# Kernel optimization log

Measured on AMD Instinct MI355X. Metric: run time of the kernel, lower is better.

## Reference

```python
import jax, jax.numpy as jnp
import numpy as np

N_TOKENS = 1024
HIDDEN = 2048
N_EXPERTS = 16
MOE_INTER = 1024
TOP_K = 6
N_GROUP = 4
TOPK_GROUP = 2
N_SHARED = 2
ROUTED_SCALING = 2.5
RENORM = True
CAPACITY = 1024  # >> N_TOKENS*TOP_K/N_EXPERTS = 384; overflow probability negligible


def setup_inputs() -> dict:
    key = jax.random.key(0)
    ks = jax.random.split(key, 7)
    s = 0.02
    return {
        'hidden_states': jax.random.normal(ks[0], (N_TOKENS, HIDDEN), jnp.float32),
        'gate_w': jax.random.normal(ks[1], (N_EXPERTS, HIDDEN), jnp.float32) * s,
        'gate_bias': jax.random.normal(ks[2], (N_EXPERTS,), jnp.float32) * s,
        'w_gate_up': jax.random.normal(ks[3], (N_EXPERTS, HIDDEN, 2 * MOE_INTER), jnp.float32) * s,
        'w_down': jax.random.normal(ks[4], (N_EXPERTS, MOE_INTER, HIDDEN), jnp.float32) * s,
        'shared_w_gate_up': jax.random.normal(ks[5], (HIDDEN, 2 * N_SHARED * MOE_INTER), jnp.float32) * s,
        'shared_w_down': jax.random.normal(ks[6], (N_SHARED * MOE_INTER, HIDDEN), jnp.float32) * s,
    }


def _swiglu(gu):
    # npu_swiglu with activate_left=True: silu(first half) * second half
    g, u = jnp.split(gu, 2, axis=-1)
    return jax.nn.silu(g) * u


def reference(hidden_states, gate_w, gate_bias, w_gate_up, w_down, shared_w_gate_up, shared_w_down):
    x = hidden_states
    N, H = x.shape
    E, K, C = N_EXPERTS, TOP_K, CAPACITY
    P = N * K  # number of (token, slot) pairs

    # ---- MoEGate: router logits + noaux_tc grouped top-k ----
    logits = x @ gate_w.T                              # [N, E]
    scores = jax.nn.sigmoid(logits)                    # sigmoid scoring (noaux_tc)
    s_corr = scores + gate_bias[None, :]
    sg = s_corr.reshape(N, N_GROUP, E // N_GROUP)
    group_scores = jax.lax.top_k(sg, 2)[0].sum(-1)     # top-2 sum per group [N, G]
    _, gidx = jax.lax.top_k(group_scores, TOPK_GROUP)
    gmask = jnp.sum(jax.nn.one_hot(gidx, N_GROUP, dtype=jnp.float32), axis=1) > 0
    masked = jnp.where(gmask[:, :, None], sg, -jnp.inf).reshape(N, E)
    _, topk_ids = jax.lax.top_k(masked, K)             # [N, K]
    w = jnp.take_along_axis(scores, topk_ids, axis=-1)  # weights from original scores
    if RENORM:
        w = w / jnp.sum(w, axis=-1, keepdims=True)
    w = w * ROUTED_SCALING

    # ---- dispatch: fixed-capacity buffers per expert ----
    flat_e = topk_ids.reshape(P)
    onehot = jax.nn.one_hot(flat_e, E, dtype=jnp.int32)
    pos = jnp.cumsum(onehot, axis=0)[jnp.arange(P), flat_e] - 1  # slot within expert
    valid = pos < C
    buf = jnp.full((E, C), P, jnp.int32).at[flat_e, jnp.clip(pos, 0, C - 1)].set(
        jnp.where(valid, jnp.arange(P, dtype=jnp.int32), P))
    tok = jnp.where(buf < P, buf // K, N)              # token index per slot, N = pad
    x_pad = jnp.concatenate([x, jnp.zeros((1, H), x.dtype)], axis=0)
    xe = x_pad[tok]                                    # [E, C, H]

    # ---- grouped expert GEMMs (SwiGLU MLP per expert) ----
    h = jnp.einsum('ech,ehi->eci', xe, w_gate_up)      # [E, C, 2I]
    y = jnp.einsum('eci,eih->ech', _swiglu(h), w_down)  # [E, C, H]

    # ---- combine: weighted scatter-add back to tokens ----
    w_pad = jnp.concatenate([w.reshape(P), jnp.zeros((1,), w.dtype)])
    pw = w_pad[jnp.where(buf < P, buf, P)]             # [E, C]
    routed = jnp.zeros((N + 1, H), x.dtype).at[tok].add(y * pw[:, :, None])[:N]

    # ---- shared experts (reduce_results=False, fused add) ----
    shared = _swiglu(x @ shared_w_gate_up) @ shared_w_down
    return routed + shared
```

## Files before the change

### kernel.cpp

```cpp
#include <hip/hip_runtime.h>
#include <hip/hip_bf16.h>
#include <math.h>

typedef __attribute__((ext_vector_type(8))) short bf16x8;
typedef __attribute__((ext_vector_type(4))) float f32x4;

#define N_TOK 1024
#define HID   2048
#define NEXP  16
#define NE2   18
#define INTER 1024
#define TOPK  6
#define CAP   1024

__device__ __forceinline__ unsigned short f2bf(float f) {
  unsigned u = __builtin_bit_cast(unsigned, f);
  u += 0x7fffu + ((u >> 16) & 1u);
  return (unsigned short)(u >> 16);
}
__device__ __forceinline__ float b2f(short s) {
  unsigned u = ((unsigned)(unsigned short)s) << 16;
  return __builtin_bit_cast(float, u);
}
__device__ __forceinline__ void gll16(const void* g, void* l) {
  __builtin_amdgcn_global_load_lds(
      (const __attribute__((address_space(1))) unsigned int*)g,
      (__attribute__((address_space(3))) unsigned int*)l, 16, 0, 0);
}
__device__ __forceinline__ void xcd_remap(int& bx, int& by, int& bz) {
  int gx = gridDim.x, gy = gridDim.y;
  int nwg = gx * gy * (int)gridDim.z;
  int lid = bx + gx * (by + gy * bz);
  int q = nwg >> 3, r = nwg & 7;
  int xcd = lid & 7, i = lid >> 3;
  int swz = (xcd < r ? xcd * (q + 1) : r * (q + 1) + (xcd - r) * q) + i;
  bx = swz % gx; int t2 = swz / gx; by = t2 % gy; bz = t2 / gy;
}

__global__ __launch_bounds__(256) void router_k(
    const float* __restrict__ x, const float* __restrict__ gw,
    const float* __restrict__ gb, int* __restrict__ counts,
    int* __restrict__ tok_list, int* __restrict__ meta,
    float* __restrict__ pwt, unsigned short* __restrict__ x_bf)
{
  const int t   = blockIdx.x;
  const int tid = threadIdx.x;
  __shared__ float xrow[HID];
  __shared__ float logits[NEXP];

  for (int i = tid; i < HID; i += 256) {
    float v = x[(size_t)t * HID + i];
    xrow[i] = v;
    x_bf[(size_t)t * HID + i] = f2bf(v);
  }
  __syncthreads();

  const int w = tid >> 6, lane = tid & 63;
  for (int s = 0; s < 4; ++s) {
    int e = w * 4 + s;
    const float* g = gw + (size_t)e * HID;
    float p = 0.f;
    for (int i = lane; i < HID; i += 64) p += xrow[i] * g[i];
    for (int off = 32; off; off >>= 1) p += __shfl_down(p, off);
    if (lane == 0) logits[e] = p;
  }
  __syncthreads();

  if (tid == 0) {
    float sc[NEXP], scorr[NEXP];
    for (int e = 0; e < NEXP; ++e) {
      float s1 = 1.f / (1.f + expf(-logits[e]));
      sc[e] = s1; scorr[e] = s1 + gb[e];
    }
    float gs[4];
    for (int g = 0; g < 4; ++g) {
      float m1 = -1e30f, m2 = -1e30f;
      for (int j = 0; j < 4; ++j) {
        float v = scorr[g * 4 + j];
        if (v > m1) { m2 = m1; m1 = v; } else if (v > m2) m2 = v;
      }
      gs[g] = m1 + m2;
    }
    int g1 = 0;
    for (int g = 1; g < 4; ++g) if (gs[g] > gs[g1]) g1 = g;
    int g2 = -1;
    for (int g = 0; g < 4; ++g) { if (g == g1) continue; if (g2 < 0 || gs[g] > gs[g2]) g2 = g; }

    bool taken[NEXP];
    for (int e = 0; e < NEXP; ++e) taken[e] = false;
    int ids[TOPK]; float wv[TOPK]; float wsum = 0.f;
    for (int k = 0; k < TOPK; ++k) {
      int best = -1; float bv = -1e30f;
      for (int e = 0; e < NEXP; ++e) {
        int grp = e >> 2;
        if (grp != g1 && grp != g2) continue;
        if (taken[e]) continue;
        if (scorr[e] > bv) { bv = scorr[e]; best = e; }
      }
      taken[best] = true; ids[k] = best; wv[k] = sc[best]; wsum += sc[best];
    }
    float inv = 2.5f / wsum;
    for (int k = 0; k < TOPK; ++k) {
      int e = ids[k];
      int slot = atomicAdd(&counts[e], 1);
      tok_list[e * CAP + slot] = t;
      meta[t * TOPK + k] = (e << 16) | slot;
      pwt[t * TOPK + k] = wv[k] * inv;
    }
  }
}

__global__ __launch_bounds__(256) void t_gu_k(
    const float* __restrict__ wgu, const float* __restrict__ sgu,
    unsigned short* __restrict__ dst)
{
  const int z = blockIdx.z;
  const int n0 = blockIdx.x * 64, k0 = blockIdx.y * 64;
  const float* src; int ld; int cb;
  if (z < 16) { src = wgu + (size_t)z * HID * (2 * INTER); ld = 2 * INTER; cb = n0; }
  else { int j = z - 16; src = sgu; ld = 4096;
         cb = (n0 < 1024) ? j * 1024 + n0 : 1024 * j + 1024 + n0; }
  __shared__ __align__(16) unsigned short t2[64][72];
  const int tid = threadIdx.x;
  const int kb = tid >> 4, nb = tid & 15;
  unsigned short h[4][4];
  #pragma unroll
  for (int j = 0; j < 4; ++j) {
    float4 f = *(const float4*)(src + (size_t)(k0 + kb * 4 + j) * ld + cb + nb * 4);
    h[j][0] = f2bf(f.x); h[j][1] = f2bf(f.y); h[j][2] = f2bf(f.z); h[j][3] = f2bf(f.w);
  }
  #pragma unroll
  for (int i = 0; i < 4; ++i) {
    int rr = nb * 4 + i;
    unsigned lo  = h[0][i] | ((unsigned)h[1][i] << 16);
    unsigned hi2 = h[2][i] | ((unsigned)h[3][i] << 16);
    unsigned long long v = (unsigned long long)lo | ((unsigned long long)hi2 << 32);
    *(unsigned long long*)((char*)t2 + rr * 144 + ((kb * 8) ^ ((rr & 7) << 4))) = v;
  }
  __syncthreads();
  unsigned short* d = dst + (size_t)z * HID * (2 * INTER);
  #pragma unroll
  for (int i = 0; i < 2; ++i) {
    int c = tid + 256 * i;
    int nl = c >> 3, s = c & 7;
    uint4 v = *(const uint4*)((const char*)t2 + nl * 144 + ((s * 16) ^ ((nl & 7) << 4)));
    *(uint4*)(d + (size_t)(n0 + nl) * HID + k0 + s * 8) = v;
  }
}

__global__ __launch_bounds__(256) void t_d_k(
    const float* __restrict__ wd, const float* __restrict__ sd,
    unsigned short* __restrict__ dst)
{
  const int z = blockIdx.z;
  const int n0 = blockIdx.x * 64, k0 = blockIdx.y * 64;
  const float* src = (z < 16) ? wd + (size_t)z * INTER * HID
                              : sd + (size_t)(z - 16) * INTER * HID;
  __shared__ __align__(16) unsigned short t2[64][72];
  const int tid = threadIdx.x;
  const int kb = tid >> 4, nb = tid & 15;
  unsigned short h[4][4];
  #pragma unroll
  for (int j = 0; j < 4; ++j) {
    float4 f = *(const float4*)(src + (size_t)(k0 + kb * 4 + j) * HID + n0 + nb * 4);
    h[j][0] = f2bf(f.x); h[j][1] = f2bf(f.y); h[j][2] = f2bf(f.z); h[j][3] = f2bf(f.w);
  }
  #pragma unroll
  for (int i = 0; i < 4; ++i) {
    int rr = nb * 4 + i;
    unsigned lo  = h[0][i] | ((unsigned)h[1][i] << 16);
    unsigned hi2 = h[2][i] | ((unsigned)h[3][i] << 16);
    unsigned long long v = (unsigned long long)lo | ((unsigned long long)hi2 << 32);
    *(unsigned long long*)((char*)t2 + rr * 144 + ((kb * 8) ^ ((rr & 7) << 4))) = v;
  }
  __syncthreads();
  unsigned short* d = dst + (size_t)z * HID * INTER;
  #pragma unroll
  for (int i = 0; i < 2; ++i) {
    int c = tid + 256 * i;
    int nl = c >> 3, s = c & 7;
    uint4 v = *(const uint4*)((const char*)t2 + nl * 144 + ((s * 16) ^ ((nl & 7) << 4)));
    *(uint4*)(d + (size_t)(n0 + nl) * INTER + k0 + s * 8) = v;
  }
}

template<int MODE>
__global__ __launch_bounds__(256) void gemm_bf16_k(
    const unsigned short* __restrict__ A, int lda, size_t a_estride,
    const unsigned short* __restrict__ Wt, int K, size_t w_estride,
    const int* __restrict__ counts, const int* __restrict__ tok_list,
    unsigned short* __restrict__ outb, int out_ld, size_t out_estride)
{
  int bx = blockIdx.x, by = blockIdx.y, bz = blockIdx.z;
  xcd_remap(bx, by, bz);
  const int e  = bz;
  const int m0 = by * 128;
  const int M  = (e < 16) ? counts[e] : N_TOK;
  if (m0 >= M) return;
  const int n0 = bx * (MODE == 0 ? 64 : 128);

  __shared__ __align__(16) unsigned short Al[128 * 64];
  __shared__ __align__(16) unsigned short Bl[128 * 64];

  const int tid = threadIdx.x, lane = tid & 63, wid = tid >> 6;
  const int wm = wid >> 1, wn = wid & 1, l15 = lane & 15, hi = lane >> 4;

  const unsigned short* Ap = A + (size_t)e * a_estride;
  const unsigned short* Wp = Wt + (size_t)e * w_estride;

  const unsigned short* asrc[4]; void* adst[4];
  const unsigned short* bsrc[4]; void* bdst[4];
  #pragma unroll
  for (int i = 0; i < 4; ++i) {
    int c = tid + 256 * i;
    int r = c >> 3, s = c & 7, sl = s ^ (r & 7);
    int slot = m0 + r;
    int row;
    if (MODE == 0) row = (e < 16) ? ((slot < M) ? tok_list[e * CAP + slot] : 0) : slot;
    else           row = slot;
    asrc[i] = Ap + (size_t)row * lda + sl * 8;
    adst[i] = (char*)Al + c * 16;
    int nrow = (MODE == 0) ? ((r < 64) ? n0 + r : 1024 + n0 + (r - 64)) : (n0 + r);
    bsrc[i] = Wp + (size_t)nrow * K + sl * 8;
    bdst[i] = (char*)Bl + c * 16;
  }

  int bn[4];
  if (MODE == 0) { bn[0] = wn*32; bn[1] = wn*32+16; bn[2] = 64+wn*32; bn[3] = 80+wn*32; }
  else           { bn[0] = wn*64; bn[1] = wn*64+16; bn[2] = wn*64+32; bn[3] = wn*64+48; }

  f32x4 acc[4][4];
  #pragma unroll
  for (int a0 = 0; a0 < 4; ++a0)
    #pragma unroll
    for (int b0 = 0; b0 < 4; ++b0) acc[a0][b0] = (f32x4){0.f, 0.f, 0.f, 0.f};

  for (int kt = 0; kt < K; kt += 64) {
    #pragma unroll
    for (int i = 0; i < 4; ++i) gll16(asrc[i] + kt, adst[i]);
    #pragma unroll
    for (int i = 0; i < 4; ++i) gll16(bsrc[i] + kt, bdst[i]);
    __syncthreads();

    #pragma unroll
    for (int kk = 0; kk < 64; kk += 32) {
      bf16x8 af[4], bv[4];
      #pragma unroll
      for (int mi = 0; mi < 4; ++mi) {
        int r = wm * 64 + mi * 16 + l15;
        int off = (r * 128 + (kk + hi * 8) * 2) ^ ((r & 7) << 4);
        af[mi] = *(const bf16x8*)((const char*)Al + off);
      }
      #pragma unroll
      for (int ni = 0; ni < 4; ++ni) {
        int r = bn[ni] + l15;
        int off = (r * 128 + (kk + hi * 8) * 2) ^ ((r & 7) << 4);
        bv[ni] = *(const bf16x8*)((const char*)Bl + off);
      }
      #pragma unroll
      for (int mi = 0; mi < 4; ++mi)
        #pragma unroll
        for (int ni = 0; ni < 4; ++ni)
          acc[mi][ni] = __builtin_amdgcn_mfma_f32_16x16x32_bf16(af[mi], bv[ni], acc[mi][ni], 0, 0, 0);
    }
    __syncthreads();
  }

  const int rbase = hi * 4;
  if (MODE == 0) {
    #pragma unroll
    for (int mi = 0; mi < 4; ++mi)
      #pragma unroll
      for (int rr = 0; rr < 4; ++rr) {
        int slot = m0 + wm * 64 + mi * 16 + rbase + rr;
        if (slot >= M) continue;
        #pragma unroll
        for (int j = 0; j < 2; ++j) {
          float g = acc[mi][j][rr], u = acc[mi][j + 2][rr];
          float sv = g / (1.f + expf(-g)) * u;
          int col = n0 + wn * 32 + j * 16 + l15;
          outb[(size_t)e * out_estride + (size_t)slot * out_ld + col] = f2bf(sv);
        }
      }
  } else {
    #pragma unroll
    for (int mi = 0; mi < 4; ++mi)
      #pragma unroll
      for (int rr = 0; rr < 4; ++rr) {
        int slot = m0 + wm * 64 + mi * 16 + rbase + rr;
        if (slot >= M) continue;
        unsigned short* row = outb + (size_t)e * out_estride + (size_t)slot * out_ld;
        #pragma unroll
        for (int ni = 0; ni < 4; ++ni)
          row[n0 + bn[ni] + l15] = f2bf(acc[mi][ni][rr]);
      }
  }
}

__global__ __launch_bounds__(256) void combine_k(
    const unsigned short* __restrict__ ybuf, const int* __restrict__ meta,
    const float* __restrict__ pwt, float* __restrict__ out)
{
  const int t = blockIdx.x;
  const int c0 = threadIdx.x * 8;
  float acc[8];
  {
    bf16x8 v0 = *(const bf16x8*)(ybuf + ((size_t)16 * CAP + t) * HID + c0);
    bf16x8 v1 = *(const bf16x8*)(ybuf + ((size_t)17 * CAP + t) * HID + c0);
    #pragma unroll
    for (int j = 0; j < 8; ++j) acc[j] = b2f(v0[j]) + b2f(v1[j]);
  }
  #pragma unroll
  for (int k = 0; k < TOPK; ++k) {
    int m = meta[t * TOPK + k];
    float w = pwt[t * TOPK + k];
    int e = m >> 16, s = m & 0xffff;
    bf16x8 v = *(const bf16x8*)(ybuf + ((size_t)e * CAP + s) * HID + c0);
    #pragma unroll
    for (int j = 0; j < 8; ++j) acc[j] += w * b2f(v[j]);
  }
  float4* o = (float4*)(out + (size_t)t * HID + c0);
  o[0] = make_float4(acc[0], acc[1], acc[2], acc[3]);
  o[1] = make_float4(acc[4], acc[5], acc[6], acc[7]);
}

extern "C" void kernel_launch(void* const* d_in, const int* in_sizes, int n_in,
                              void* d_out, int out_size, void* d_ws, size_t ws_size,
                              hipStream_t stream) {
  const float* x   = (const float*)d_in[0];
  const float* gw  = (const float*)d_in[1];
  const float* gb  = (const float*)d_in[2];
  const float* wgu = (const float*)d_in[3];
  const float* wd  = (const float*)d_in[4];
  const float* sgu = (const float*)d_in[5];
  const float* sd  = (const float*)d_in[6];
  float* out = (float*)d_out;

  char* ws = (char*)d_ws;
  int*   counts   = (int*)ws;
  int*   tok_list = (int*)(ws + 256);
  int*   meta     = (int*)(ws + 256 + 65536);
  float* pwt      = (float*)(ws + 256 + 65536 + 24576);
  unsigned short* x_bf  = (unsigned short*)(ws + 128 * 1024);
  unsigned short* act   = x_bf + (size_t)N_TOK * HID;
  unsigned short* ybuf  = act + (size_t)NE2 * CAP * INTER;
  unsigned short* wt_gu = ybuf + (size_t)NE2 * CAP * HID;
  unsigned short* wt_d  = wt_gu + (size_t)NE2 * HID * 2 * INTER;
  const size_t need = (size_t)((char*)(wt_d + (size_t)NE2 * HID * INTER) - ws);
  if (ws_size < need) return;

  hipMemsetAsync(counts, 0, 256, stream);
  router_k<<<N_TOK, 256, 0, stream>>>(x, gw, gb, counts, tok_list, meta, pwt, x_bf);

  t_gu_k<<<dim3(2 * INTER / 64, HID / 64, NE2), 256, 0, stream>>>(wgu, sgu, wt_gu);
  t_d_k<<<dim3(HID / 64, INTER / 64, NE2), 256, 0, stream>>>(wd, sd, wt_d);

  gemm_bf16_k<0><<<dim3(INTER / 64, CAP / 128, NE2), 256, 0, stream>>>(
      x_bf, HID, 0, wt_gu, HID, (size_t)HID * 2 * INTER, counts, tok_list,
      act, INTER, (size_t)CAP * INTER);
  gemm_bf16_k<1><<<dim3(HID / 128, CAP / 128, NE2), 256, 0, stream>>>(
      act, INTER, (size_t)CAP * INTER, wt_d, INTER, (size_t)HID * INTER, counts, nullptr,
      ybuf, HID, (size_t)CAP * HID);

  combine_k<<<N_TOK, 256, 0, stream>>>(ybuf, meta, pwt, out);
}
```

Measured before the change: 478.3 us.

## Widen GEMM N-tile and double-buffer weight tiles in LDS

The grouped expert GEMMs now use a 128x256 output tile (twice as wide in N) with 32 accumulators per lane. The weight (B) tiles are double-buffered in LDS so the next tile's global-to-LDS loads overlap with MFMA work on the current one, while A is still single-buffered and reloaded after a barrier. The XCD block remapping is removed and launch bounds ask for 2 blocks per SM. The goal is more reuse of the A tile per weight load and less load latency exposed at barriers, at the cost of more LDS (about 80KB), higher register pressure, and fewer blocks in flight.

```diff
diff --git a/kernel.cpp b/kernel.cpp
--- a/kernel.cpp
+++ b/kernel.cpp
@@ -26,15 +26,6 @@
   __builtin_amdgcn_global_load_lds(
       (const __attribute__((address_space(1))) unsigned int*)g,
       (__attribute__((address_space(3))) unsigned int*)l, 16, 0, 0);
-}
-__device__ __forceinline__ void xcd_remap(int& bx, int& by, int& bz) {
-  int gx = gridDim.x, gy = gridDim.y;
-  int nwg = gx * gy * (int)gridDim.z;
-  int lid = bx + gx * (by + gy * bz);
-  int q = nwg >> 3, r = nwg & 7;
-  int xcd = lid & 7, i = lid >> 3;
-  int swz = (xcd < r ? xcd * (q + 1) : r * (q + 1) + (xcd - r) * q) + i;
-  bx = swz % gx; int t2 = swz / gx; by = t2 % gy; bz = t2 / gy;
 }
 
 __global__ __launch_bounds__(256) void router_k(
@@ -185,22 +176,20 @@
 }
 
 template<int MODE>
-__global__ __launch_bounds__(256) void gemm_bf16_k(
+__global__ __launch_bounds__(256, 2) void gemm_bf16_k(
     const unsigned short* __restrict__ A, int lda, size_t a_estride,
     const unsigned short* __restrict__ Wt, int K, size_t w_estride,
     const int* __restrict__ counts, const int* __restrict__ tok_list,
     unsigned short* __restrict__ outb, int out_ld, size_t out_estride)
 {
-  int bx = blockIdx.x, by = blockIdx.y, bz = blockIdx.z;
-  xcd_remap(bx, by, bz);
-  const int e  = bz;
-  const int m0 = by * 128;
+  const int e  = blockIdx.z;
+  const int m0 = blockIdx.y * 128;
   const int M  = (e < 16) ? counts[e] : N_TOK;
   if (m0 >= M) return;
-  const int n0 = bx * (MODE == 0 ? 64 : 128);
+  const int n0 = blockIdx.x * (MODE == 0 ? 128 : 256);
 
   __shared__ __align__(16) unsigned short Al[128 * 64];
-  __shared__ __align__(16) unsigned short Bl[128 * 64];
+  __shared__ __align__(16) unsigned short Bl[2][256 * 64];
 
   const int tid = threadIdx.x, lane = tid & 63, wid = tid >> 6;
   const int wm = wid >> 1, wn = wid & 1, l15 = lane & 15, hi = lane >> 4;
@@ -208,63 +197,98 @@
   const unsigned short* Ap = A + (size_t)e * a_estride;
   const unsigned short* Wp = Wt + (size_t)e * w_estride;
 
-  const unsigned short* asrc[4]; void* adst[4];
-  const unsigned short* bsrc[4]; void* bdst[4];
+  const int r0 = tid >> 3, s0 = tid & 7, sl = s0 ^ (r0 & 7);
+  const unsigned short* asrc[4]; int aoff[4];
   #pragma unroll
   for (int i = 0; i < 4; ++i) {
-    int c = tid + 256 * i;
-    int r = c >> 3, s = c & 7, sl = s ^ (r & 7);
+    int r = r0 + 32 * i;
     int slot = m0 + r;
     int row;
     if (MODE == 0) row = (e < 16) ? ((slot < M) ? tok_list[e * CAP + slot] : 0) : slot;
     else           row = slot;
     asrc[i] = Ap + (size_t)row * lda + sl * 8;
-    adst[i] = (char*)Al + c * 16;
-    int nrow = (MODE == 0) ? ((r < 64) ? n0 + r : 1024 + n0 + (r - 64)) : (n0 + r);
-    bsrc[i] = Wp + (size_t)nrow * K + sl * 8;
-    bdst[i] = (char*)Bl + c * 16;
-  }
-
-  int bn[4];
-  if (MODE == 0) { bn[0] = wn*32; bn[1] = wn*32+16; bn[2] = 64+wn*32; bn[3] = 80+wn*32; }
-  else           { bn[0] = wn*64; bn[1] = wn*64+16; bn[2] = wn*64+32; bn[3] = wn*64+48; }
-
-  f32x4 acc[4][4];
+    aoff[i] = (tid + 256 * i) * 16;
+  }
+  const unsigned short* bpg;
+  const unsigned short* bpu;
+  if (MODE == 0) {
+    bpg = Wp + (size_t)(n0 + r0) * K + sl * 8;
+    bpu = Wp + (size_t)(1024 + n0 + r0) * K + sl * 8;
+  } else {
+    bpg = Wp + (size_t)(n0 + r0) * K + sl * 8;
+    bpu = bpg + (size_t)128 * K;
+  }
+  const size_t bstep = (size_t)32 * K;
+
+  int bn[8];
+  #pragma unroll
+  for (int ni = 0; ni < 8; ++ni) {
+    if (MODE == 0) bn[ni] = (ni < 4) ? (wn * 64 + ni * 16) : (128 + wn * 64 + (ni - 4) * 16);
+    else           bn[ni] = wn * 128 + ni * 16;
+  }
+
+  f32x4 acc[4][8];
   #pragma unroll
   for (int a0 = 0; a0 < 4; ++a0)
     #pragma unroll
-    for (int b0 = 0; b0 < 4; ++b0) acc[a0][b0] = (f32x4){0.f, 0.f, 0.f, 0.f};
-
-  for (int kt = 0; kt < K; kt += 64) {
-    #pragma unroll
-    for (int i = 0; i < 4; ++i) gll16(asrc[i] + kt, adst[i]);
-    #pragma unroll
-    for (int i = 0; i < 4; ++i) gll16(bsrc[i] + kt, bdst[i]);
-    __syncthreads();
-
-    #pragma unroll
-    for (int kk = 0; kk < 64; kk += 32) {
-      bf16x8 af[4], bv[4];
-      #pragma unroll
-      for (int mi = 0; mi < 4; ++mi) {
-        int r = wm * 64 + mi * 16 + l15;
-        int off = (r * 128 + (kk + hi * 8) * 2) ^ ((r & 7) << 4);
-        af[mi] = *(const bf16x8*)((const char*)Al + off);
-      }
-      #pragma unroll
-      for (int ni = 0; ni < 4; ++ni) {
-        int r = bn[ni] + l15;
-        int off = (r * 128 + (kk + hi * 8) * 2) ^ ((r & 7) << 4);
-        bv[ni] = *(const bf16x8*)((const char*)Bl + off);
-      }
-      #pragma unroll
-      for (int mi = 0; mi < 4; ++mi)
-        #pragma unroll
-        for (int ni = 0; ni < 4; ++ni)
-          acc[mi][ni] = __builtin_amdgcn_mfma_f32_16x16x32_bf16(af[mi], bv[ni], acc[mi][ni], 0, 0, 0);
-    }
-    __syncthreads();
-  }
+    for (int b0 = 0; b0 < 8; ++b0) acc[a0][b0] = (f32x4){0.f, 0.f, 0.f, 0.f};
+
+  #define ISSUE_B(buf, kt)                                                  \
+    _Pragma("unroll")                                                       \
+    for (int i = 0; i < 4; ++i)                                             \
+      gll16(bpg + bstep * i + (kt), (char*)(buf) + (tid + 256 * i) * 16);   \
+    _Pragma("unroll")                                                       \
+    for (int i = 0; i < 4; ++i)                                             \
+      gll16(bpu + bstep * i + (kt), (char*)(buf) + (tid + 256 * (i + 4)) * 16);
+  #define ISSUE_A(kt)                                                       \
+    _Pragma("unroll")                                                       \
+    for (int i = 0; i < 4; ++i) gll16(asrc[i] + (kt), (char*)Al + aoff[i]);
+  #define COMPUTE(Bb)                                                       \
+    _Pragma("unroll")                                                       \
+    for (int kk = 0; kk < 64; kk += 32) {                                   \
+      bf16x8 af[4], bv[8];                                                  \
+      _Pragma("unroll")                                                     \
+      for (int mi = 0; mi < 4; ++mi) {                                      \
+        int r = wm * 64 + mi * 16 + l15;                                    \
+        int off = (r * 128 + (kk + hi * 8) * 2) ^ ((r & 7) << 4);           \
+        af[mi] = *(const bf16x8*)((const char*)Al + off);                   \
+      }                                                                     \
+      _Pragma("unroll")                                                     \
+      for (int ni = 0; ni < 8; ++ni) {                                      \
+        int r = bn[ni] + l15;                                               \
+        int off = (r * 128 + (kk + hi * 8) * 2) ^ ((r & 7) << 4);           \
+        bv[ni] = *(const bf16x8*)((const char*)(Bb) + off);                 \
+      }                                                                     \
+      _Pragma("unroll")                                                     \
+      for (int mi = 0; mi < 4; ++mi)                                        \
+        _Pragma("unroll")                                                   \
+        for (int ni = 0; ni < 8; ++ni)                                      \
+          acc[mi][ni] = __builtin_amdgcn_mfma_f32_16x16x32_bf16(            \
+              af[mi], bv[ni], acc[mi][ni], 0, 0, 0);                        \
+    }
+
+  const int nt = K >> 6;
+  ISSUE_B(Bl[0], 0)
+  ISSUE_A(0)
+  asm volatile("s_waitcnt vmcnt(0)" ::: "memory");
+  __builtin_amdgcn_s_barrier();
+
+  int p = 0;
+  for (int t = 0; t < nt; ++t) {
+    const bool pf = (t + 1 < nt);
+    if (pf) { ISSUE_B(Bl[p ^ 1], (t + 1) << 6) }
+    COMPUTE(Bl[p])
+    __builtin_amdgcn_s_barrier();
+    if (pf) {
+      ISSUE_A((t + 1) << 6)
+      asm volatile("s_waitcnt vmcnt(0)" ::: "memory");
+      __builtin_amdgcn_s_barrier();
+    }
+    p ^= 1;
+  }
+  #undef ISSUE_B
+  #undef ISSUE_A
+  #undef COMPUTE
 
   const int rbase = hi * 4;
   if (MODE == 0) {
@@ -275,10 +299,10 @@
         int slot = m0 + wm * 64 + mi * 16 + rbase + rr;
         if (slot >= M) continue;
         #pragma unroll
-        for (int j = 0; j < 2; ++j) {
-          float g = acc[mi][j][rr], u = acc[mi][j + 2][rr];
+        for (int ni = 0; ni < 4; ++ni) {
+          float g = acc[mi][ni][rr], u = acc[mi][ni + 4][rr];
           float sv = g / (1.f + expf(-g)) * u;
-          int col = n0 + wn * 32 + j * 16 + l15;
+          int col = n0 + wn * 64 + ni * 16 + l15;
           outb[(size_t)e * out_estride + (size_t)slot * out_ld + col] = f2bf(sv);
         }
       }
@@ -291,7 +315,7 @@
         if (slot >= M) continue;
         unsigned short* row = outb + (size_t)e * out_estride + (size_t)slot * out_ld;
         #pragma unroll
-        for (int ni = 0; ni < 4; ++ni)
+        for (int ni = 0; ni < 8; ++ni)
           row[n0 + bn[ni] + l15] = f2bf(acc[mi][ni][rr]);
       }
   }
@@ -355,10 +379,10 @@
   t_gu_k<<<dim3(2 * INTER / 64, HID / 64, NE2), 256, 0, stream>>>(wgu, sgu, wt_gu);
   t_d_k<<<dim3(HID / 64, INTER / 64, NE2), 256, 0, stream>>>(wd, sd, wt_d);
 
-  gemm_bf16_k<0><<<dim3(INTER / 64, CAP / 128, NE2), 256, 0, stream>>>(
+  gemm_bf16_k<0><<<dim3(INTER / 128, CAP / 128, NE2), 256, 0, stream>>>(
       x_bf, HID, 0, wt_gu, HID, (size_t)HID * 2 * INTER, counts, tok_list,
       act, INTER, (size_t)CAP * INTER);
-  gemm_bf16_k<1><<<dim3(HID / 128, CAP / 128, NE2), 256, 0, stream>>>(
+  gemm_bf16_k<1><<<dim3(HID / 256, CAP / 128, NE2), 256, 0, stream>>>(
       act, INTER, (size_t)CAP * INTER, wt_d, INTER, (size_t)HID * INTER, counts, nullptr,
       ybuf, HID, (size_t)CAP * HID);
 
```

Result: no change. 484.9 us (+1.4%).
